# Kernel tuning notes

Measured on AMD Instinct MI355X. Metric: run time of the kernel, lower is better.

Reference implementation:

```python
import jax, jax.numpy as jnp
import numpy as np

INPUT_DIM = 66
OUTPUT_COUNT = 8192
NUM_PAIRS = 65536

def setup_inputs() -> dict:
    key = jax.random.key(0)
    k1, k2, k3, k4 = jax.random.split(key, 4)
    x = jax.random.normal(k1, (NUM_PAIRS, INPUT_DIM), dtype=jnp.float32)
    query = jax.random.normal(k2, (OUTPUT_COUNT, INPUT_DIM), dtype=jnp.float32)
    # nn.Linear(input_dim, input_dim): weight [out,in], bias [out]
    bound = 1.0 / np.sqrt(INPUT_DIM)
    Wk = jax.random.uniform(k3, (INPUT_DIM, INPUT_DIM), minval=-bound, maxval=bound, dtype=jnp.float32)
    bk = jax.random.uniform(k4, (INPUT_DIM,), minval=-bound, maxval=bound, dtype=jnp.float32)
    return {"x": x, "query": query, "Wk": Wk, "bk": bk}

def reference(x, query, Wk, bk):
    # K = Linear(x): x @ Wk^T + bk  -> [num_pairs, d]
    K = x @ Wk.T + bk
    # scores: [output_count, num_pairs]
    scores = jnp.einsum("qd,nd->qn", query, K)
    attn = jax.nn.softmax(scores, axis=1)
    # selected: [output_count, d] — note values are raw x, not K
    selected = attn @ x
    return selected
```

## Files before the change

kernel.cpp:

```cpp
#include <hip/hip_runtime.h>
#include <cstdint>


typedef __bf16    bf16x4 __attribute__((ext_vector_type(4)));
typedef __bf16    bf16x8 __attribute__((ext_vector_type(8)));
typedef _Float16  f16x4  __attribute__((ext_vector_type(4)));
typedef _Float16  f16x8  __attribute__((ext_vector_type(8)));
typedef float     f32x16 __attribute__((ext_vector_type(16)));

extern "C" __device__ float __ocml_native_exp2_f32(float);

#define NUM_PAIRS   65536
#define NUM_Q       8192
#define DIM         66
#define QPITCH      80
#define KFT         2560
#define XFT         3072
#define PARTP       68
#define NTILES      (NUM_PAIRS/32)

__device__ __forceinline__ f32x16 mfma_bf16(bf16x8 a, bf16x8 b, f32x16 c) {
    return __builtin_amdgcn_mfma_f32_32x32x16_bf16(a, b, c, 0, 0, 0);
}
__device__ __forceinline__ f32x16 mfma_f16(f16x8 a, f16x8 b, f32x16 c) {
    return __builtin_amdgcn_mfma_f32_32x32x16_f16(a, b, c, 0, 0, 0);
}
__device__ __forceinline__ void plswap(unsigned &a, unsigned &b) {
    asm("v_permlane32_swap_b32 %0, %1" : "+v"(a), "+v"(b));
}
__device__ __forceinline__ unsigned packbf(float a, float b) {
    union { __bf16 h[2]; unsigned u; } t;
    t.h[0] = (__bf16)a; t.h[1] = (__bf16)b;
    return t.u;
}
union U4 { unsigned u[4]; bf16x8 v; };

__device__ __forceinline__ void makefrags(const f32x16 &s, U4 *f) {
    float P[16];
    #pragma unroll
    for (int r = 0; r < 16; ++r) P[r] = __ocml_native_exp2_f32(s[r]);
    unsigned E0 = packbf(P[0],  P[1]),  E1 = packbf(P[2],  P[3]);
    unsigned F0 = packbf(P[4],  P[5]),  F1 = packbf(P[6],  P[7]);
    plswap(E0, F0); plswap(E1, F1);
    f[0].u[0] = E0; f[0].u[1] = E1; f[0].u[2] = F0; f[0].u[3] = F1;
    unsigned G0 = packbf(P[8],  P[9]),  G1 = packbf(P[10], P[11]);
    unsigned H0 = packbf(P[12], P[13]), H1 = packbf(P[14], P[15]);
    plswap(G0, H0); plswap(G1, H1);
    f[1].u[0] = G0; f[1].u[1] = G1; f[1].u[2] = H0; f[1].u[3] = H1;
}

__device__ __forceinline__ void compute_tile(const f16x8 (&kc)[5], const __bf16* __restrict__ xp,
                                             const f16x8 (&aQ)[2][5], f32x16 (&o)[2][3]) {
    bf16x8 xa[6];
    #pragma unroll
    for (int c = 0; c < 6; ++c) xa[c] = *(const bf16x8*)(xp + c * 512);
    f32x16 s0 = {}, s1 = {};
    #pragma unroll
    for (int kk = 0; kk < 5; ++kk) {
        s0 = mfma_f16(kc[kk], aQ[0][kk], s0);
        s1 = mfma_f16(kc[kk], aQ[1][kk], s1);
    }
    U4 f0[2], f1[2];
    makefrags(s0, f0);
    makefrags(s1, f1);
    #pragma unroll
    for (int par = 0; par < 2; ++par)
        #pragma unroll
        for (int dt = 0; dt < 3; ++dt) {
            o[0][dt] = mfma_bf16(f0[par].v, xa[par * 3 + dt], o[0][dt]);
            o[1][dt] = mfma_bf16(f1[par].v, xa[par * 3 + dt], o[1][dt]);
        }
}

#define PAP 104
#define SKP 88
__global__ __launch_bounds__(256) void prep_kernel(
    const float* __restrict__ x, const float* __restrict__ query,
    const float* __restrict__ Wk, const float* __restrict__ bk,
    unsigned short* __restrict__ Kf_u, unsigned short* __restrict__ Xf_u,
    unsigned short* __restrict__ Qh_u) {
    const int tid = threadIdx.x;
    if (blockIdx.x >= 512) {
        _Float16* Qh = (_Float16*)Qh_u;
        int base = (blockIdx.x - 512) * 1280;
        #pragma unroll
        for (int k = 0; k < 5; ++k) {
            int idx = base + k * 256 + tid;
            int q = idx / QPITCH, c = idx % QPITCH;
            float v = (c < DIM) ? query[(long)q * DIM + c] * 1.4426950408889634f : 0.f;
            Qh[idx] = (_Float16)v;
        }
        return;
    }
    _Float16* Kf = (_Float16*)Kf_u;
    __bf16*   Xf = (__bf16*)Xf_u;
    __shared__ _Float16 sxh[128 * PAP];
    __shared__ _Float16 sW[96 * PAP];
    __shared__ _Float16 sK[128 * SKP];
    const long n0 = (long)blockIdx.x * 128;

    for (int i = tid; i < 128 * 96; i += 256) {
        int r = i / 96, c = i % 96;
        sxh[r * PAP + c] = (_Float16)((c < DIM) ? x[(n0 + r) * DIM + c] : 0.f);
    }
    for (int i = tid; i < 96 * 96; i += 256) {
        int cc = i / 96, d = i % 96;
        sW[cc * PAP + d] = (_Float16)((cc < DIM && d < DIM) ? Wk[cc * DIM + d] : 0.f);
    }
    __syncthreads();

    const int lane = tid & 63, w = tid >> 6;
    const int l31 = lane & 31, h = lane >> 5;

    #pragma unroll
    for (int nt = 0; nt < 3; ++nt) {
        f32x16 acc = {};
        #pragma unroll
        for (int kk = 0; kk < 6; ++kk) {
            f16x8 a = *(const f16x8*)&sxh[(w * 32 + l31) * PAP + kk * 16 + h * 8];
            f16x8 b = *(const f16x8*)&sW[(nt * 32 + l31) * PAP + kk * 16 + h * 8];
            acc = mfma_f16(a, b, acc);
        }
        int c = nt * 32 + l31;
        float bkv = (c < DIM) ? bk[c] : 0.f;
        if (c < SKP) {
            #pragma unroll
            for (int r = 0; r < 16; ++r) {
                int row = (r & 3) + 8 * (r >> 2) + 4 * h;
                sK[(w * 32 + row) * SKP + c] = (_Float16)(acc[r] + bkv);
            }
        }
    }
    __syncthreads();

    for (int i = 0; i < 5; ++i) {
        int slot = i * 256 + tid;
        int tt = slot / 320, rem = slot % 320;
        int kk = rem / 64, l = rem % 64;
        const _Float16* src = &sK[(32 * tt + (l & 31)) * SKP + kk * 16 + (l >> 5) * 8];
        f16x4 lo = *(const f16x4*)src;
        f16x4 hi = *(const f16x4*)(src + 4);
        f16x8 v = __builtin_shufflevector(lo, hi, 0, 1, 2, 3, 4, 5, 6, 7);
        *(f16x8*)&Kf[((long)blockIdx.x * 4 + tt) * KFT + kk * 512 + l * 8] = v;
    }
    for (int i = 0; i < 6; ++i) {
        int slot = i * 256 + tid;
        int tt = slot / 384, rem = slot % 384;
        int c = rem / 64, l = rem % 64;
        int dt = c % 3, par = c / 3;
        int d = 32 * dt + (l & 31);
        int p0 = 32 * tt + 16 * par + 8 * (l >> 5);
        bf16x8 v;
        #pragma unroll
        for (int j = 0; j < 8; ++j) {
            float vv = 0.f;
            if (d < DIM) vv = (float)sxh[(p0 + j) * PAP + d];
            else if (d == DIM) vv = 1.f;
            v[j] = (__bf16)vv;
        }
        *(bf16x8*)&Xf[((long)blockIdx.x * 4 + tt) * XFT + c * 512 + l * 8] = v;
    }
}

__global__ __launch_bounds__(256, 2) void flash_kernel(
    const unsigned short* __restrict__ Qh_u, const unsigned short* __restrict__ Kf_u,
    const unsigned short* __restrict__ Xf_u, float* __restrict__ Part, int NS) {
    const _Float16* Qh = (const _Float16*)Qh_u;
    const _Float16* Kf = (const _Float16*)Kf_u;
    const __bf16*   Xf = (const __bf16*)Xf_u;

    const int tid = threadIdx.x;
    const int lane = tid & 63, wave = tid >> 6;
    const int l31 = lane & 31, h = lane >> 5;
    const int qb = blockIdx.x / NS, ns = blockIdx.x % NS;
    const int tiles = NTILES / NS;
    const int qbase = qb * 256 + wave * 64;

    const _Float16* kf = Kf + (long)(ns * tiles) * KFT + lane * 8;
    const __bf16*   xf = Xf + (long)(ns * tiles) * XFT + lane * 8;

    f16x8 aQ[2][5];
    #pragma unroll
    for (int qt = 0; qt < 2; ++qt)
        #pragma unroll
        for (int kk = 0; kk < 5; ++kk)
            aQ[qt][kk] = *(const f16x8*)&Qh[(long)(qbase + qt * 32 + l31) * QPITCH + kk * 16 + h * 8];

    f32x16 o[2][3] = {};

    f16x8 kA[5], kB[5];
    #pragma unroll
    for (int kk = 0; kk < 5; ++kk) kA[kk] = *(const f16x8*)(kf + kk * 512);

    for (int t = 0; t < tiles; t += 2) {
        if ((t & 31) == 0) asm volatile("s_barrier");
        {
            const _Float16* kp = kf + (long)(t + 1) * KFT;
            #pragma unroll
            for (int kk = 0; kk < 5; ++kk) kB[kk] = *(const f16x8*)(kp + kk * 512);
        }
        compute_tile(kA, xf + (long)t * XFT, aQ, o);
        if (t + 2 < tiles) {
            const _Float16* kp = kf + (long)(t + 2) * KFT;
            #pragma unroll
            for (int kk = 0; kk < 5; ++kk) kA[kk] = *(const f16x8*)(kp + kk * 512);
        }
        compute_tile(kB, xf + (long)(t + 1) * XFT, aQ, o);
    }

    #pragma unroll
    for (int qt = 0; qt < 2; ++qt)
        #pragma unroll
        for (int dt = 0; dt < 3; ++dt)
            #pragma unroll
            for (int r = 0; r < 16; ++r) {
                int row = (r & 3) + 8 * (r >> 2) + 4 * h;
                int q = qbase + qt * 32 + row;
                int d = dt * 32 + l31;
                if (d < DIM + 1)
                    Part[((long)q * NS + ns) * PARTP + d] = o[qt][dt][r];
            }
}

__global__ __launch_bounds__(256) void combine_kernel(
    const float* __restrict__ Part, float* __restrict__ out, int NS) {
    int q = blockIdx.x * 2 + (threadIdx.x >> 7);
    int d = threadIdx.x & 127;
    if (d >= DIM) return;
    const float* base = Part + (long)q * NS * PARTP;
    float num = 0.f, den = 0.f;
    #pragma unroll 4
    for (int s = 0; s < NS; ++s) {
        num += base[s * PARTP + d];
        den += base[s * PARTP + DIM];
    }
    out[(long)q * DIM + d] = num / den;
}

extern "C" void kernel_launch(void* const* d_in, const int* in_sizes, int n_in,
                              void* d_out, int out_size, void* d_ws, size_t ws_size,
                              hipStream_t stream) {
    const float* x     = (const float*)d_in[0];
    const float* query = (const float*)d_in[1];
    const float* Wk    = (const float*)d_in[2];
    const float* bk    = (const float*)d_in[3];
    float* out = (float*)d_out;
    char* ws = (char*)d_ws;

    unsigned short* Qh = (unsigned short*)(ws + 0);
    unsigned short* Kf = (unsigned short*)(ws + 1310720);
    unsigned short* Xf = (unsigned short*)(ws + 11796480);
    float* Part        = (float*)(ws + 24379392);

    int NS = 16;
    while (NS > 1 &&
           24379392ULL + (unsigned long long)NS * NUM_Q * PARTP * 4ULL > (unsigned long long)ws_size)
        NS >>= 1;

    prep_kernel<<<1024, 256, 0, stream>>>(x, query, Wk, bk, Kf, Xf, Qh);
    flash_kernel<<<(NUM_Q / 256) * NS, 256, 0, stream>>>(Qh, Kf, Xf, Part, NS);
    combine_kernel<<<NUM_Q / 2, 256, 0, stream>>>(Part, out, NS);
}
```

Before: 280.1 us.

## Prefetch X tiles in register double-buffer and reduce splits via atomics

Loads the X value fragments for the next tile together with the K fragments, so both are double-buffered in registers ahead of the MFMA work instead of being loaded inside each tile. It also replaces the per-split partial buffer and combine kernel with float atomicAdd into a single accumulator that is zeroed by a memset, followed by a light normalization kernel. This removes the partial-buffer write/read traffic. In exchange it adds register pressure, atomic contention across 16 splits, and non-deterministic summation order.

Measured after the change: 302.6 us. 8.0% more time.

```diff
diff --git a/kernel.cpp b/kernel.cpp
--- a/kernel.cpp
+++ b/kernel.cpp
@@ -16,7 +16,7 @@
 #define QPITCH      80
 #define KFT         2560
 #define XFT         3072
-#define PARTP       68
+#define ACCP        68
 #define NTILES      (NUM_PAIRS/32)
 
 __device__ __forceinline__ f32x16 mfma_bf16(bf16x8 a, bf16x8 b, f32x16 c) {
@@ -49,11 +49,8 @@
     f[1].u[0] = G0; f[1].u[1] = G1; f[1].u[2] = H0; f[1].u[3] = H1;
 }
 
-__device__ __forceinline__ void compute_tile(const f16x8 (&kc)[5], const __bf16* __restrict__ xp,
+__device__ __forceinline__ void compute_tile(const f16x8 (&kc)[5], const bf16x8 (&xa)[6],
                                              const f16x8 (&aQ)[2][5], f32x16 (&o)[2][3]) {
-    bf16x8 xa[6];
-    #pragma unroll
-    for (int c = 0; c < 6; ++c) xa[c] = *(const bf16x8*)(xp + c * 512);
     f32x16 s0 = {}, s1 = {};
     #pragma unroll
     for (int kk = 0; kk < 5; ++kk) {
@@ -164,7 +161,7 @@
 
 __global__ __launch_bounds__(256, 2) void flash_kernel(
     const unsigned short* __restrict__ Qh_u, const unsigned short* __restrict__ Kf_u,
-    const unsigned short* __restrict__ Xf_u, float* __restrict__ Part, int NS) {
+    const unsigned short* __restrict__ Xf_u, float* __restrict__ Acc, int NS) {
     const _Float16* Qh = (const _Float16*)Qh_u;
     const _Float16* Kf = (const _Float16*)Kf_u;
     const __bf16*   Xf = (const __bf16*)Xf_u;
@@ -188,24 +185,33 @@
 
     f32x16 o[2][3] = {};
 
-    f16x8 kA[5], kB[5];
+    f16x8  kA[5], kB[5];
+    bf16x8 xA[6], xB[6];
     #pragma unroll
     for (int kk = 0; kk < 5; ++kk) kA[kk] = *(const f16x8*)(kf + kk * 512);
+    #pragma unroll
+    for (int c = 0; c < 6; ++c)    xA[c]  = *(const bf16x8*)(xf + c * 512);
 
     for (int t = 0; t < tiles; t += 2) {
         if ((t & 31) == 0) asm volatile("s_barrier");
         {
             const _Float16* kp = kf + (long)(t + 1) * KFT;
+            const __bf16*   xp = xf + (long)(t + 1) * XFT;
             #pragma unroll
             for (int kk = 0; kk < 5; ++kk) kB[kk] = *(const f16x8*)(kp + kk * 512);
-        }
-        compute_tile(kA, xf + (long)t * XFT, aQ, o);
+            #pragma unroll
+            for (int c = 0; c < 6; ++c)    xB[c]  = *(const bf16x8*)(xp + c * 512);
+        }
+        compute_tile(kA, xA, aQ, o);
         if (t + 2 < tiles) {
             const _Float16* kp = kf + (long)(t + 2) * KFT;
+            const __bf16*   xp = xf + (long)(t + 2) * XFT;
             #pragma unroll
             for (int kk = 0; kk < 5; ++kk) kA[kk] = *(const f16x8*)(kp + kk * 512);
-        }
-        compute_tile(kB, xf + (long)(t + 1) * XFT, aQ, o);
+            #pragma unroll
+            for (int c = 0; c < 6; ++c)    xA[c]  = *(const bf16x8*)(xp + c * 512);
+        }
+        compute_tile(kB, xB, aQ, o);
     }
 
     #pragma unroll
@@ -218,23 +224,16 @@
                 int q = qbase + qt * 32 + row;
                 int d = dt * 32 + l31;
                 if (d < DIM + 1)
-                    Part[((long)q * NS + ns) * PARTP + d] = o[qt][dt][r];
+                    atomicAdd(&Acc[(long)q * ACCP + d], o[qt][dt][r]);
             }
 }
 
-__global__ __launch_bounds__(256) void combine_kernel(
-    const float* __restrict__ Part, float* __restrict__ out, int NS) {
-    int q = blockIdx.x * 2 + (threadIdx.x >> 7);
-    int d = threadIdx.x & 127;
-    if (d >= DIM) return;
-    const float* base = Part + (long)q * NS * PARTP;
-    float num = 0.f, den = 0.f;
-    #pragma unroll 4
-    for (int s = 0; s < NS; ++s) {
-        num += base[s * PARTP + d];
-        den += base[s * PARTP + DIM];
-    }
-    out[(long)q * DIM + d] = num / den;
+__global__ __launch_bounds__(256) void norm_kernel(
+    const float* __restrict__ Acc, float* __restrict__ out) {
+    int idx = blockIdx.x * 256 + threadIdx.x;
+    if (idx >= NUM_Q * DIM) return;
+    int q = idx / DIM, d = idx - q * DIM;
+    out[idx] = Acc[q * ACCP + d] / Acc[q * ACCP + DIM];
 }
 
 extern "C" void kernel_launch(void* const* d_in, const int* in_sizes, int n_in,
@@ -250,14 +249,12 @@
     unsigned short* Qh = (unsigned short*)(ws + 0);
     unsigned short* Kf = (unsigned short*)(ws + 1310720);
     unsigned short* Xf = (unsigned short*)(ws + 11796480);
-    float* Part        = (float*)(ws + 24379392);
-
-    int NS = 16;
-    while (NS > 1 &&
-           24379392ULL + (unsigned long long)NS * NUM_Q * PARTP * 4ULL > (unsigned long long)ws_size)
-        NS >>= 1;
-
+    float* Acc         = (float*)(ws + 24379392);
+
+    const int NS = 16;
+
+    hipMemsetAsync(Acc, 0, (size_t)NUM_Q * ACCP * 4, stream);
     prep_kernel<<<1024, 256, 0, stream>>>(x, query, Wk, bk, Kf, Xf, Qh);
-    flash_kernel<<<(NUM_Q / 256) * NS, 256, 0, stream>>>(Qh, Kf, Xf, Part, NS);
-    combine_kernel<<<NUM_Q / 2, 256, 0, stream>>>(Part, out, NS);
-}
+    flash_kernel<<<(NUM_Q / 256) * NS, 256, 0, stream>>>(Qh, Kf, Xf, Acc, NS);
+    norm_kernel<<<(NUM_Q * DIM + 255) / 256, 256, 0, stream>>>(Acc, out);
+}
```

## Stagger wave tile order and double-buffer X fragments in flash loop

Applied to the files above, without the earlier changes.

Each wave now starts its sweep over the key/value tiles at a different offset and wraps around, so the four waves in a block no longer request the same tiles from memory at the same moment. The periodic s_barrier that kept the waves in lockstep is removed. X fragments are now prefetched into registers alongside the K fragments, one tile ahead. NS is fixed at 16 with no workspace-size check. The extra X buffers raise register pressure, and fixing NS can overflow the workspace if it is smaller than expected.

New measurement: 296.8 us. +5.9%, slower.

```diff
diff --git a/kernel.cpp b/kernel.cpp
--- a/kernel.cpp
+++ b/kernel.cpp
@@ -49,11 +49,8 @@
     f[1].u[0] = G0; f[1].u[1] = G1; f[1].u[2] = H0; f[1].u[3] = H1;
 }
 
-__device__ __forceinline__ void compute_tile(const f16x8 (&kc)[5], const __bf16* __restrict__ xp,
+__device__ __forceinline__ void compute_tile(const f16x8 (&kc)[5], const bf16x8 (&xa)[6],
                                              const f16x8 (&aQ)[2][5], f32x16 (&o)[2][3]) {
-    bf16x8 xa[6];
-    #pragma unroll
-    for (int c = 0; c < 6; ++c) xa[c] = *(const bf16x8*)(xp + c * 512);
     f32x16 s0 = {}, s1 = {};
     #pragma unroll
     for (int kk = 0; kk < 5; ++kk) {
@@ -174,7 +171,9 @@
     const int l31 = lane & 31, h = lane >> 5;
     const int qb = blockIdx.x / NS, ns = blockIdx.x % NS;
     const int tiles = NTILES / NS;
+    const int tmask = tiles - 1;
     const int qbase = qb * 256 + wave * 64;
+    const int slip = wave * (tiles >> 2);
 
     const _Float16* kf = Kf + (long)(ns * tiles) * KFT + lane * 8;
     const __bf16*   xf = Xf + (long)(ns * tiles) * XFT + lane * 8;
@@ -188,24 +187,38 @@
 
     f32x16 o[2][3] = {};
 
-    f16x8 kA[5], kB[5];
-    #pragma unroll
-    for (int kk = 0; kk < 5; ++kk) kA[kk] = *(const f16x8*)(kf + kk * 512);
-
-    for (int t = 0; t < tiles; t += 2) {
-        if ((t & 31) == 0) asm volatile("s_barrier");
+    f16x8  kA[5], kB[5];
+    bf16x8 xA[6], xB[6];
+    {
+        const _Float16* kp = kf + (long)slip * KFT;
+        const __bf16*   xp = xf + (long)slip * XFT;
+        #pragma unroll
+        for (int kk = 0; kk < 5; ++kk) kA[kk] = *(const f16x8*)(kp + kk * 512);
+        #pragma unroll
+        for (int c = 0; c < 6; ++c)    xA[c]  = *(const bf16x8*)(xp + c * 512);
+    }
+
+    for (int i = 0; i < tiles; i += 2) {
         {
-            const _Float16* kp = kf + (long)(t + 1) * KFT;
+            int t1 = (slip + i + 1) & tmask;
+            const _Float16* kp = kf + (long)t1 * KFT;
+            const __bf16*   xp = xf + (long)t1 * XFT;
             #pragma unroll
             for (int kk = 0; kk < 5; ++kk) kB[kk] = *(const f16x8*)(kp + kk * 512);
-        }
-        compute_tile(kA, xf + (long)t * XFT, aQ, o);
-        if (t + 2 < tiles) {
-            const _Float16* kp = kf + (long)(t + 2) * KFT;
+            #pragma unroll
+            for (int c = 0; c < 6; ++c)    xB[c]  = *(const bf16x8*)(xp + c * 512);
+        }
+        compute_tile(kA, xA, aQ, o);
+        {
+            int t2 = (slip + i + 2) & tmask;
+            const _Float16* kp = kf + (long)t2 * KFT;
+            const __bf16*   xp = xf + (long)t2 * XFT;
             #pragma unroll
             for (int kk = 0; kk < 5; ++kk) kA[kk] = *(const f16x8*)(kp + kk * 512);
-        }
-        compute_tile(kB, xf + (long)(t + 1) * XFT, aQ, o);
+            #pragma unroll
+            for (int c = 0; c < 6; ++c)    xA[c]  = *(const bf16x8*)(xp + c * 512);
+        }
+        compute_tile(kB, xB, aQ, o);
     }
 
     #pragma unroll
@@ -252,10 +265,7 @@
     unsigned short* Xf = (unsigned short*)(ws + 11796480);
     float* Part        = (float*)(ws + 24379392);
 
-    int NS = 16;
-    while (NS > 1 &&
-           24379392ULL + (unsigned long long)NS * NUM_Q * PARTP * 4ULL > (unsigned long long)ws_size)
-        NS >>= 1;
+    const int NS = 16;
 
     prep_kernel<<<1024, 256, 0, stream>>>(x, query, Wk, bk, Kf, Xf, Qh);
     flash_kernel<<<(NUM_Q / 256) * NS, 256, 0, stream>>>(Qh, Kf, Xf, Part, NS);
```

## Fold key projection into queries and prefetch X fragments in flash loop

Applied to the files above, without the earlier changes.

Uses softmax shift invariance to drop the key bias and computes Wk^T·q per query in the prep kernel. Raw x then serves directly as the key operand, which removes the per-pair key-projection MFMA GEMM and its shared-memory staging. The flash loop now double-buffers the X value fragments in registers alongside the K fragments and drops the periodic s_barrier. It also hardcodes 16 splits without checking workspace size, and the extra registers could put pressure on occupancy.

After: 279.8 us. No clear change (-0.1%).

```diff
diff --git a/kernel.cpp b/kernel.cpp
--- a/kernel.cpp
+++ b/kernel.cpp
@@ -49,11 +49,8 @@
     f[1].u[0] = G0; f[1].u[1] = G1; f[1].u[2] = H0; f[1].u[3] = H1;
 }
 
-__device__ __forceinline__ void compute_tile(const f16x8 (&kc)[5], const __bf16* __restrict__ xp,
+__device__ __forceinline__ void compute_tile(const f16x8 (&kc)[5], const bf16x8 (&xa)[6],
                                              const f16x8 (&aQ)[2][5], f32x16 (&o)[2][3]) {
-    bf16x8 xa[6];
-    #pragma unroll
-    for (int c = 0; c < 6; ++c) xa[c] = *(const bf16x8*)(xp + c * 512);
     f32x16 s0 = {}, s1 = {};
     #pragma unroll
     for (int kk = 0; kk < 5; ++kk) {
@@ -73,63 +70,45 @@
 }
 
 #define PAP 104
-#define SKP 88
+#define WQP 67
 __global__ __launch_bounds__(256) void prep_kernel(
     const float* __restrict__ x, const float* __restrict__ query,
-    const float* __restrict__ Wk, const float* __restrict__ bk,
-    unsigned short* __restrict__ Kf_u, unsigned short* __restrict__ Xf_u,
+    const float* __restrict__ Wk,
+    unsigned short* __restrict__ Af_u, unsigned short* __restrict__ Xf_u,
     unsigned short* __restrict__ Qh_u) {
     const int tid = threadIdx.x;
     if (blockIdx.x >= 512) {
+        __shared__ float sWq[DIM * WQP];
+        __shared__ float sq[16 * WQP];
         _Float16* Qh = (_Float16*)Qh_u;
-        int base = (blockIdx.x - 512) * 1280;
-        #pragma unroll
-        for (int k = 0; k < 5; ++k) {
-            int idx = base + k * 256 + tid;
-            int q = idx / QPITCH, c = idx % QPITCH;
-            float v = (c < DIM) ? query[(long)q * DIM + c] * 1.4426950408889634f : 0.f;
-            Qh[idx] = (_Float16)v;
+        const int q0 = (blockIdx.x - 512) * 16;
+        for (int i = tid; i < DIM * DIM; i += 256)
+            sWq[(i % DIM) * WQP + (i / DIM)] = Wk[i];
+        for (int i = tid; i < 16 * DIM; i += 256)
+            sq[(i / DIM) * WQP + (i % DIM)] = query[(long)(q0 + i / DIM) * DIM + (i % DIM)];
+        __syncthreads();
+        for (int slot = tid; slot < 16 * QPITCH; slot += 256) {
+            int qi = slot / QPITCH, c = slot % QPITCH;
+            float acc = 0.f;
+            if (c < DIM) {
+                const float* qr = &sq[qi * WQP];
+                const float* wr = &sWq[c * WQP];
+                #pragma unroll 6
+                for (int d = 0; d < DIM; ++d) acc += qr[d] * wr[d];
+                acc *= 1.4426950408889634f;
+            }
+            Qh[(long)(q0 + qi) * QPITCH + c] = (_Float16)acc;
         }
         return;
     }
-    _Float16* Kf = (_Float16*)Kf_u;
+    _Float16* Af = (_Float16*)Af_u;
     __bf16*   Xf = (__bf16*)Xf_u;
     __shared__ _Float16 sxh[128 * PAP];
-    __shared__ _Float16 sW[96 * PAP];
-    __shared__ _Float16 sK[128 * SKP];
     const long n0 = (long)blockIdx.x * 128;
 
     for (int i = tid; i < 128 * 96; i += 256) {
         int r = i / 96, c = i % 96;
         sxh[r * PAP + c] = (_Float16)((c < DIM) ? x[(n0 + r) * DIM + c] : 0.f);
-    }
-    for (int i = tid; i < 96 * 96; i += 256) {
-        int cc = i / 96, d = i % 96;
-        sW[cc * PAP + d] = (_Float16)((cc < DIM && d < DIM) ? Wk[cc * DIM + d] : 0.f);
-    }
-    __syncthreads();
-
-    const int lane = tid & 63, w = tid >> 6;
-    const int l31 = lane & 31, h = lane >> 5;
-
-    #pragma unroll
-    for (int nt = 0; nt < 3; ++nt) {
-        f32x16 acc = {};
-        #pragma unroll
-        for (int kk = 0; kk < 6; ++kk) {
-            f16x8 a = *(const f16x8*)&sxh[(w * 32 + l31) * PAP + kk * 16 + h * 8];
-            f16x8 b = *(const f16x8*)&sW[(nt * 32 + l31) * PAP + kk * 16 + h * 8];
-            acc = mfma_f16(a, b, acc);
-        }
-        int c = nt * 32 + l31;
-        float bkv = (c < DIM) ? bk[c] : 0.f;
-        if (c < SKP) {
-            #pragma unroll
-            for (int r = 0; r < 16; ++r) {
-                int row = (r & 3) + 8 * (r >> 2) + 4 * h;
-                sK[(w * 32 + row) * SKP + c] = (_Float16)(acc[r] + bkv);
-            }
-        }
     }
     __syncthreads();
 
@@ -137,11 +116,11 @@
         int slot = i * 256 + tid;
         int tt = slot / 320, rem = slot % 320;
         int kk = rem / 64, l = rem % 64;
-        const _Float16* src = &sK[(32 * tt + (l & 31)) * SKP + kk * 16 + (l >> 5) * 8];
+        const _Float16* src = &sxh[(32 * tt + (l & 31)) * PAP + kk * 16 + (l >> 5) * 8];
         f16x4 lo = *(const f16x4*)src;
         f16x4 hi = *(const f16x4*)(src + 4);
         f16x8 v = __builtin_shufflevector(lo, hi, 0, 1, 2, 3, 4, 5, 6, 7);
-        *(f16x8*)&Kf[((long)blockIdx.x * 4 + tt) * KFT + kk * 512 + l * 8] = v;
+        *(f16x8*)&Af[((long)blockIdx.x * 4 + tt) * KFT + kk * 512 + l * 8] = v;
     }
     for (int i = 0; i < 6; ++i) {
         int slot = i * 256 + tid;
@@ -163,10 +142,10 @@
 }
 
 __global__ __launch_bounds__(256, 2) void flash_kernel(
-    const unsigned short* __restrict__ Qh_u, const unsigned short* __restrict__ Kf_u,
+    const unsigned short* __restrict__ Qh_u, const unsigned short* __restrict__ Af_u,
     const unsigned short* __restrict__ Xf_u, float* __restrict__ Part, int NS) {
     const _Float16* Qh = (const _Float16*)Qh_u;
-    const _Float16* Kf = (const _Float16*)Kf_u;
+    const _Float16* Af = (const _Float16*)Af_u;
     const __bf16*   Xf = (const __bf16*)Xf_u;
 
     const int tid = threadIdx.x;
@@ -176,7 +155,7 @@
     const int tiles = NTILES / NS;
     const int qbase = qb * 256 + wave * 64;
 
-    const _Float16* kf = Kf + (long)(ns * tiles) * KFT + lane * 8;
+    const _Float16* kf = Af + (long)(ns * tiles) * KFT + lane * 8;
     const __bf16*   xf = Xf + (long)(ns * tiles) * XFT + lane * 8;
 
     f16x8 aQ[2][5];
@@ -188,24 +167,32 @@
 
     f32x16 o[2][3] = {};
 
-    f16x8 kA[5], kB[5];
+    f16x8  kA[5], kB[5];
+    bf16x8 xA[6], xB[6];
     #pragma unroll
     for (int kk = 0; kk < 5; ++kk) kA[kk] = *(const f16x8*)(kf + kk * 512);
+    #pragma unroll
+    for (int c = 0; c < 6; ++c)    xA[c]  = *(const bf16x8*)(xf + c * 512);
 
     for (int t = 0; t < tiles; t += 2) {
-        if ((t & 31) == 0) asm volatile("s_barrier");
         {
             const _Float16* kp = kf + (long)(t + 1) * KFT;
+            const __bf16*   xp = xf + (long)(t + 1) * XFT;
             #pragma unroll
             for (int kk = 0; kk < 5; ++kk) kB[kk] = *(const f16x8*)(kp + kk * 512);
-        }
-        compute_tile(kA, xf + (long)t * XFT, aQ, o);
+            #pragma unroll
+            for (int c = 0; c < 6; ++c)    xB[c]  = *(const bf16x8*)(xp + c * 512);
+        }
+        compute_tile(kA, xA, aQ, o);
         if (t + 2 < tiles) {
             const _Float16* kp = kf + (long)(t + 2) * KFT;
+            const __bf16*   xp = xf + (long)(t + 2) * XFT;
             #pragma unroll
             for (int kk = 0; kk < 5; ++kk) kA[kk] = *(const f16x8*)(kp + kk * 512);
-        }
-        compute_tile(kB, xf + (long)(t + 1) * XFT, aQ, o);
+            #pragma unroll
+            for (int c = 0; c < 6; ++c)    xA[c]  = *(const bf16x8*)(xp + c * 512);
+        }
+        compute_tile(kB, xB, aQ, o);
     }
 
     #pragma unroll
@@ -243,21 +230,17 @@
     const float* x     = (const float*)d_in[0];
     const float* query = (const float*)d_in[1];
     const float* Wk    = (const float*)d_in[2];
-    const float* bk    = (const float*)d_in[3];
     float* out = (float*)d_out;
     char* ws = (char*)d_ws;
 
     unsigned short* Qh = (unsigned short*)(ws + 0);
-    unsigned short* Kf = (unsigned short*)(ws + 1310720);
+    unsigned short* Af = (unsigned short*)(ws + 1310720);
     unsigned short* Xf = (unsigned short*)(ws + 11796480);
     float* Part        = (float*)(ws + 24379392);
 
-    int NS = 16;
-    while (NS > 1 &&
-           24379392ULL + (unsigned long long)NS * NUM_Q * PARTP * 4ULL > (unsigned long long)ws_size)
-        NS >>= 1;
-
-    prep_kernel<<<1024, 256, 0, stream>>>(x, query, Wk, bk, Kf, Xf, Qh);
-    flash_kernel<<<(NUM_Q / 256) * NS, 256, 0, stream>>>(Qh, Kf, Xf, Part, NS);
+    const int NS = 16;
+
+    prep_kernel<<<1024, 256, 0, stream>>>(x, query, Wk, Af, Xf, Qh);
+    flash_kernel<<<(NUM_Q / 256) * NS, 256, 0, stream>>>(Qh, Af, Xf, Part, NS);
     combine_kernel<<<NUM_Q / 2, 256, 0, stream>>>(Part, out, NS);
 }
```
